# Optimization experiments

Hardware: AMD Instinct MI355X
Metric: run time of the kernel (lower is better)

Reference implementation:

```python
import jax, jax.numpy as jnp
import numpy as np

B, S, D, H, DFF = 2, 2048, 1024, 16, 4096
DK = D // H
EPS = float(np.finfo(np.float32).eps)  # torch RMSNorm default eps = finfo eps


def rmsnorm(x, g):
    var = jnp.mean(x * x, axis=-1, keepdims=True)
    return x * jax.lax.rsqrt(var + EPS) * g


def rope_cos_sin(seq_len, dim, base=10000.0):
    inv_freq = 1.0 / (base ** (jnp.arange(0, dim, 2, dtype=jnp.float32) / dim))
    t = jnp.arange(seq_len, dtype=jnp.float32)
    freqs = jnp.outer(t, inv_freq)            # [S, dim/2]
    emb = jnp.concatenate([freqs, freqs], -1)  # [S, dim]
    return jnp.cos(emb), jnp.sin(emb)


def rotate_half(x):
    x1, x2 = x[..., : x.shape[-1] // 2], x[..., x.shape[-1] // 2:]
    return jnp.concatenate([-x2, x1], axis=-1)


def setup_inputs() -> dict:
    key = jax.random.key(0)
    ks = jax.random.split(key, 16)
    sc = 0.02
    return {
        "x": jax.random.normal(ks[0], (B, S, D), jnp.float32),
        "wq": jax.random.normal(ks[1], (D, D), jnp.float32) * sc,
        "bq": jnp.zeros((D,), jnp.float32),
        "wk": jax.random.normal(ks[2], (D, D), jnp.float32) * sc,
        "bk": jnp.zeros((D,), jnp.float32),
        "wv": jax.random.normal(ks[3], (D, D), jnp.float32) * sc,
        "bv": jnp.zeros((D,), jnp.float32),
        "wo": jax.random.normal(ks[4], (D, D), jnp.float32) * sc,
        "bo": jnp.zeros((D,), jnp.float32),
        "w1": jax.random.normal(ks[5], (D, DFF), jnp.float32) * sc,
        "b1": jnp.zeros((DFF,), jnp.float32),
        "w2": jax.random.normal(ks[6], (DFF, D), jnp.float32) * sc,
        "b2": jnp.zeros((D,), jnp.float32),
        "g1": jnp.ones((D,), jnp.float32),
        "g2": jnp.ones((D,), jnp.float32),
    }


def reference(x, wq, bq, wk, bk, wv, bv, wo, bo, w1, b1, w2, b2, g1, g2):
    b, s, d = x.shape
    # --- self-attention sublayer (pre-RMSNorm residual) ---
    h = rmsnorm(x, g1)
    q = (h @ wq + bq).reshape(b, s, H, DK).transpose(0, 2, 1, 3)  # [B,H,S,dk]
    k = (h @ wk + bk).reshape(b, s, H, DK).transpose(0, 2, 1, 3)
    v = (h @ wv + bv).reshape(b, s, H, DK).transpose(0, 2, 1, 3)
    cos, sin = rope_cos_sin(s, DK)
    cos = cos[None, None]  # [1,1,S,dk]
    sin = sin[None, None]
    q = q * cos + rotate_half(q) * sin
    k = k * cos + rotate_half(k) * sin
    scores = jnp.einsum("bhqd,bhkd->bhqk", q, k) / jnp.sqrt(jnp.float32(DK))
    p = jax.nn.softmax(scores, axis=-1)
    o = jnp.einsum("bhqk,bhkd->bhqd", p, v)
    o = o.transpose(0, 2, 1, 3).reshape(b, s, d)
    attn_out = o @ wo + bo
    x = x + attn_out
    # --- feed-forward sublayer ---
    h2 = rmsnorm(x, g2)
    ff = jax.nn.relu(h2 @ w1 + b1) @ w2 + b2
    return x + ff
```

## Files before the change

### kernel.cpp

```cpp
#include <hip/hip_runtime.h>
#include <math.h>

typedef unsigned short u16;
typedef __attribute__((ext_vector_type(8))) short bf16x8;
typedef __attribute__((ext_vector_type(4))) float f32x4;
typedef __attribute__((ext_vector_type(4))) unsigned int u32x4;

#define B_ 2
#define S_ 2048
#define D_ 1024
#define H_ 16
#define DK_ 64
#define DFF_ 4096
#define EPS_ 1.1920928955078125e-07f
#define EXP2SC 0.18033688011112042f

__device__ __forceinline__ float bf2f(u16 u) {
  unsigned int v = ((unsigned int)u) << 16;
  return __builtin_bit_cast(float, v);
}
__device__ __forceinline__ u16 f2bf(float f) {
  unsigned int x = __builtin_bit_cast(unsigned int, f);
  x += 0x7fffu + ((x >> 16) & 1u);
  return (u16)(x >> 16);
}

typedef __attribute__((address_space(3))) unsigned int lds_uint;
typedef const __attribute__((address_space(1))) unsigned int glb_uint;
__device__ __forceinline__ void gload16(const void* g, void* l) {
  __builtin_amdgcn_global_load_lds((glb_uint*)g, (lds_uint*)l, 16, 0, 0);
}

__device__ __forceinline__ unsigned int cvtpk(float lo, float hi) {
  unsigned int d;
  asm("v_cvt_pk_bf16_f32 %0, %1, %2" : "=v"(d) : "v"(lo), "v"(hi));
  return d;
}
__device__ __forceinline__ void plswap32(unsigned int& a, unsigned int& b) {
  asm("v_permlane32_swap_b32 %0, %1" : "+v"(a), "+v"(b));
}
__device__ __forceinline__ void plswap16(unsigned int& a, unsigned int& b) {
  asm("v_permlane16_swap_b32 %0, %1" : "+v"(a), "+v"(b));
}

__global__ __launch_bounds__(256) void rope_table(float* __restrict__ cosT,
                                                  float* __restrict__ sinT) {
  int idx = blockIdx.x * 256 + threadIdx.x;
  if (idx >= S_ * 32) return;
  int s = idx >> 5, i = idx & 31;
  double inv = exp(((double)(-2 * i) / (double)DK_) * log(10000.0));
  double ang = (double)s * inv;
  cosT[idx] = (float)cos(ang);
  sinT[idx] = (float)sin(ang);
}

__global__ __launch_bounds__(256) void convertT(const float* __restrict__ src,
                                                u16* __restrict__ dst, int R, int C) {
  __shared__ float t[32][33];
  int c0 = blockIdx.x * 32, r0 = blockIdx.y * 32;
  int tx = threadIdx.x, ty = threadIdx.y;
#pragma unroll
  for (int i = 0; i < 32; i += 8)
    t[ty + i][tx] = src[(size_t)(r0 + ty + i) * C + (c0 + tx)];
  __syncthreads();
#pragma unroll
  for (int i = 0; i < 32; i += 8)
    dst[(size_t)(c0 + ty + i) * R + (r0 + tx)] = f2bf(t[tx][ty + i]);
}

__global__ __launch_bounds__(256) void rmsnorm_k(const float* __restrict__ X,
                                                 const float* __restrict__ g,
                                                 u16* __restrict__ out) {
  const int row = blockIdx.x;
  const float* xr = X + (size_t)row * D_;
  u16* orow = out + (size_t)row * D_;
  const int tid = threadIdx.x;
  float vals[4];
  float s = 0.f;
#pragma unroll
  for (int j = 0; j < 4; j++) {
    float v = xr[tid + j * 256];
    vals[j] = v;
    s += v * v;
  }
#pragma unroll
  for (int off = 32; off > 0; off >>= 1) s += __shfl_down(s, off, 64);
  __shared__ float red[4];
  __shared__ float ssc;
  int lane = tid & 63, wave = tid >> 6;
  if (lane == 0) red[wave] = s;
  __syncthreads();
  if (tid == 0) ssc = 1.0f / sqrtf((red[0] + red[1] + red[2] + red[3]) * (1.0f / D_) + EPS_);
  __syncthreads();
  float sc = ssc;
#pragma unroll
  for (int j = 0; j < 4; j++) {
    int i = tid + j * 256;
    orow[i] = f2bf(vals[j] * sc * g[i]);
  }
}

#define GEMM_KLOOP(APTR, BPTR, KLEN, KLD)                                              \
  for (int k0 = 0; k0 < (KLEN); k0 += 64) {                                            \
    _Pragma("unroll")                                                                  \
    for (int p = 0; p < 2; p++) {                                                      \
      _Pragma("unroll")                                                                \
      for (int c = wave; c < BM / 16; c += 4) {                                        \
        const u16* gp = (APTR) + (size_t)(m0 + c * 16 + lrow) * (KLD) + k0 + p * 32 + lcol; \
        gload16(gp, (char*)As + __builtin_amdgcn_readfirstlane(p * (BM * 64) + c * 1024)); \
      }                                                                                \
      _Pragma("unroll")                                                                \
      for (int c = wave; c < BN / 16; c += 4) {                                        \
        const u16* gp = (BPTR) + (size_t)(n0 + c * 16 + lrow) * (KLD) + k0 + p * 32 + lcol; \
        gload16(gp, (char*)Bs + __builtin_amdgcn_readfirstlane(p * (BN * 64) + c * 1024)); \
      }                                                                                \
    }                                                                                  \
    __syncthreads();                                                                   \
    _Pragma("unroll")                                                                  \
    for (int p = 0; p < 2; p++) {                                                      \
      bf16x8 af[WR], bfv[WC];                                                          \
      _Pragma("unroll")                                                                \
      for (int i = 0; i < WR; i++)                                                     \
        af[i] = *(const bf16x8*)&As[p * (BM * 32) + (wm + i * 16 + l16) * 32 + quad * 8]; \
      _Pragma("unroll")                                                                \
      for (int j = 0; j < WC; j++)                                                     \
        bfv[j] = *(const bf16x8*)&Bs[p * (BN * 32) + (wn + j * 16 + l16) * 32 + quad * 8]; \
      _Pragma("unroll")                                                                \
      for (int i = 0; i < WR; i++)                                                     \
        _Pragma("unroll")                                                              \
        for (int j = 0; j < WC; j++)                                                   \
          acc[i][j] = __builtin_amdgcn_mfma_f32_16x16x32_bf16(af[i], bfv[j], acc[i][j], 0, 0, 0); \
    }                                                                                  \
    __syncthreads();                                                                   \
  }

template <int MODE, int WR, int WC>
__global__ __launch_bounds__(256) void gemm_bt(
    const u16* __restrict__ A, const u16* __restrict__ Bt, const float* __restrict__ bias,
    u16* __restrict__ outB, float* __restrict__ outF, const float* __restrict__ resF,
    int M, int N, int K) {
  constexpr int BM = 2 * WR * 16;
  constexpr int BN = 2 * WC * 16;
  __shared__ u16 As[BM * 64];
  __shared__ u16 Bs[BN * 64];
  const int tid = threadIdx.x;
  const int wave = tid >> 6, lane = tid & 63, quad = lane >> 4, l16 = lane & 15;
  const int wm = (wave >> 1) * (WR * 16), wn = (wave & 1) * (WC * 16);
  const int m0 = blockIdx.y * BM, n0 = blockIdx.x * BN;
  const int lrow = lane >> 2, lcol = (lane & 3) * 8;
  f32x4 acc[WR][WC] = {};
  GEMM_KLOOP(A, Bt, K, K)
#pragma unroll
  for (int i = 0; i < WR; i++)
#pragma unroll
    for (int j = 0; j < WC; j++) {
      int col = n0 + wn + j * 16 + l16;
      float bv = bias[col];
#pragma unroll
      for (int r = 0; r < 4; r++) {
        int row = m0 + wm + i * 16 + quad * 4 + r;
        size_t off = (size_t)row * N + col;
        float v = acc[i][j][r] + bv;
        if constexpr (MODE == 1) v = fmaxf(v, 0.f);
        if constexpr (MODE == 2) outF[off] = v + resF[off];
        else outB[off] = f2bf(v);
      }
    }
}

__global__ __launch_bounds__(256) void gemm_qkv(
    const u16* __restrict__ A, const u16* __restrict__ Bt,
    const float* __restrict__ bq, const float* __restrict__ bk, const float* __restrict__ bv,
    const float* __restrict__ cosT, const float* __restrict__ sinT,
    u16* __restrict__ Qb, u16* __restrict__ Kb, u16* __restrict__ VT, int M, int K) {
  constexpr int WR = 4, WC = 4;
  constexpr int BM = 128, BN = 128;
  __shared__ u16 As[BM * 64];
  __shared__ u16 Bs[BN * 64];
  const int tid = threadIdx.x;
  const int wave = tid >> 6, lane = tid & 63, quad = lane >> 4, l16 = lane & 15;
  const int wm = (wave >> 1) * 64, wn = (wave & 1) * 64;
  const int m0 = blockIdx.y * BM, n0 = blockIdx.x * BN;
  const int lrow = lane >> 2, lcol = (lane & 3) * 8;
  f32x4 acc[WR][WC] = {};
  GEMM_KLOOP(A, Bt, K, K)
  const int g = n0 >> 10;
  if (g < 2) {
    u16* dst = (g == 0) ? Qb : Kb;
    const float* bias = (g == 0) ? bq : bk;
    const float scq = (g == 0) ? EXP2SC : 1.0f;
#pragma unroll
    for (int i = 0; i < WR; i++)
#pragma unroll
      for (int jp = 0; jp < 2; jp++) {
        int col0 = n0 + wn + jp * 16 + l16;
        int c0 = col0 & 1023;
        float bv0 = bias[c0], bv1 = bias[c0 + 32];
        int irot = jp * 16 + l16;
        int row0 = m0 + wm + i * 16 + quad * 4;
#pragma unroll
        for (int r = 0; r < 4; r++) {
          int row = row0 + r;
          int s2 = row & 2047;
          float cs = cosT[s2 * 32 + irot];
          float sn = sinT[s2 * 32 + irot];
          float x0 = acc[i][jp][r] + bv0;
          float x1 = acc[i][jp + 2][r] + bv1;
          dst[(size_t)row * D_ + c0]      = f2bf((x0 * cs - x1 * sn) * scq);
          dst[(size_t)row * D_ + c0 + 32] = f2bf((x1 * cs + x0 * sn) * scq);
        }
      }
  } else {
#pragma unroll
    for (int i = 0; i < WR; i++)
#pragma unroll
      for (int j = 0; j < WC; j++) {
        int col = n0 + wn + j * 16 + l16;
        int c = col & 1023;
        float bvv = bv[c];
        int row0 = m0 + wm + i * 16 + quad * 4;
        int hh = c >> 6, dk = c & 63;
        int b = row0 >> 11, s2 = row0 & 2047;
        ushort4 pv;
        pv.x = f2bf(acc[i][j][0] + bvv);
        pv.y = f2bf(acc[i][j][1] + bvv);
        pv.z = f2bf(acc[i][j][2] + bvv);
        pv.w = f2bf(acc[i][j][3] + bvv);
        *(ushort4*)&VT[(((size_t)(b * H_ + hh)) * DK_ + dk) * S_ + s2] = pv;
      }
  }
}

template <int WR, int WC>
__global__ __launch_bounds__(256) void gemm_splitk(
    const u16* __restrict__ A, const u16* __restrict__ Bt, const float* __restrict__ bias,
    float* outF, int M, int N, int Kslice, int Kld) {
  constexpr int BM = 2 * WR * 16;
  constexpr int BN = 2 * WC * 16;
  __shared__ u16 As[BM * 64];
  __shared__ u16 Bs[BN * 64];
  const int tid = threadIdx.x;
  const int wave = tid >> 6, lane = tid & 63, quad = lane >> 4, l16 = lane & 15;
  const int wm = (wave >> 1) * (WR * 16), wn = (wave & 1) * (WC * 16);
  const int m0 = blockIdx.y * BM, n0 = blockIdx.x * BN;
  const int lrow = lane >> 2, lcol = (lane & 3) * 8;
  const u16* Ao = A + (size_t)blockIdx.z * Kslice;
  const u16* Bo = Bt + (size_t)blockIdx.z * Kslice;
  f32x4 acc[WR][WC] = {};
  GEMM_KLOOP(Ao, Bo, Kslice, Kld)
  const bool addb = (blockIdx.z == 0);
#pragma unroll
  for (int i = 0; i < WR; i++)
#pragma unroll
    for (int j = 0; j < WC; j++) {
      int col = n0 + wn + j * 16 + l16;
      float bv = addb ? bias[col] : 0.f;
#pragma unroll
      for (int r = 0; r < 4; r++) {
        int row = m0 + wm + i * 16 + quad * 4 + r;
        unsafeAtomicAdd(&outF[(size_t)row * N + col], acc[i][j][r] + bv);
      }
    }
}

__device__ __forceinline__ void softmax_pack(f32x4 s0, f32x4 s1, f32x4 s2, f32x4 s3,
                                             bf16x8& pf0, bf16x8& pf1) {
  f32x4 p0, p1, p2, p3;
#pragma unroll
  for (int r = 0; r < 4; r++) {
    p0[r] = exp2f(s0[r]);
    p1[r] = exp2f(s1[r]);
    p2[r] = exp2f(s2[r]);
    p3[r] = exp2f(s3[r]);
  }
  unsigned int X0 = cvtpk(p0[0], p0[1]), X1 = cvtpk(p0[2], p0[3]);
  unsigned int Y0 = cvtpk(p1[0], p1[1]), Y1 = cvtpk(p1[2], p1[3]);
  unsigned int Z0 = cvtpk(p2[0], p2[1]), Z1 = cvtpk(p2[2], p2[3]);
  unsigned int W0 = cvtpk(p3[0], p3[1]), W1 = cvtpk(p3[2], p3[3]);
  plswap32(X0, Y0); plswap16(X0, Y0);
  plswap32(X1, Y1); plswap16(X1, Y1);
  plswap32(Z0, W0); plswap16(Z0, W0);
  plswap32(Z1, W1); plswap16(Z1, W1);
  u32x4 lo = {X0, X1, Y0, Y1};
  u32x4 hi = {Z0, Z1, W0, W1};
  pf0 = __builtin_bit_cast(bf16x8, lo);
  pf1 = __builtin_bit_cast(bf16x8, hi);
}

__global__ __launch_bounds__(256, 2) void flash_attn(u16* __restrict__ Q,
                                                     const u16* __restrict__ Kg,
                                                     const u16* __restrict__ VT) {
  const int bh = blockIdx.y;
  const int b = bh >> 4, h = bh & 15;
  const int q0 = blockIdx.x * 128;
  const int tid = threadIdx.x;
  const int wave = tid >> 6, lane = tid & 63, quad = lane >> 4, l16 = lane & 15;
  const size_t base = (size_t)b * S_ * D_ + h * DK_;
  const size_t vbase = (size_t)bh * DK_ * S_;

  __shared__ u16 Ks[2][8192];
  __shared__ u16 Vts[2][8192];

  const int kkey = wave * 32 + (lane >> 3);
  const int kcol = ((lane & 7) ^ (lane >> 3)) * 8;
  const u16* kp0 = Kg + base + (size_t)kkey * D_ + kcol;
  const int vdk0 = wave * 16 + (lane >> 4);
  const int vsel = lane & 15;
  const u16* vp0 = VT + vbase + (size_t)vdk0 * S_;

#define STAGE(BU, KT)                                                                  \
  _Pragma("unroll")                                                                    \
  for (int c = 0; c < 4; c++) {                                                        \
    gload16(kp0 + (size_t)((KT) + c * 8) * D_,                                         \
            (char*)Ks + __builtin_amdgcn_readfirstlane((BU) * 16384 + wave * 4096 + c * 1024)); \
    int vdk = vdk0 + c * 4;                                                            \
    gload16(vp0 + (size_t)(c * 4) * S_ + (KT) + ((vsel ^ (vdk & 7)) * 8),              \
            (char*)Vts + __builtin_amdgcn_readfirstlane((BU) * 16384 + wave * 4096 + c * 1024)); \
  }

  STAGE(0, 0)

  const size_t qoffA = base + (size_t)(q0 + wave * 32 + l16) * D_ + quad * 8;
  const size_t qoffB = qoffA + (size_t)16 * D_;
  bf16x8 qa0 = *(const bf16x8*)(Q + qoffA);
  bf16x8 qa1 = *(const bf16x8*)(Q + qoffA + 32);
  bf16x8 qb0 = *(const bf16x8*)(Q + qoffB);
  bf16x8 qb1 = *(const bf16x8*)(Q + qoffB + 32);

  f32x4 oa[4] = {}, ob[4] = {};
  f32x4 lsa_acc = {}, lsb_acc = {};
  const u32x4 onesu = {0x3F803F80u, 0x3F803F80u, 0x3F803F80u, 0x3F803F80u};
  const bf16x8 ones = __builtin_bit_cast(bf16x8, onesu);
  const int sw = (l16 & 7) << 4;

#define TILE(BU)                                                                       \
  {                                                                                    \
    const char* KsB = (const char*)Ks + (BU) * 16384;                                  \
    const char* VtsB = (const char*)Vts + (BU) * 16384;                                \
    f32x4 sa[2][4] = {}, sb[2][4] = {};                                                \
    __builtin_amdgcn_s_setprio(1);                                                     \
    _Pragma("unroll")                                                                  \
    for (int half = 0; half < 2; half++) {                                             \
      _Pragma("unroll")                                                                \
      for (int nt = 0; nt < 4; nt++) {                                                 \
        const int kr = half * 64 + nt * 16 + l16;                                      \
        const char* krow = KsB + kr * 128;                                             \
        bf16x8 k0 = *(const bf16x8*)(krow + ((quad * 16) ^ sw));                       \
        bf16x8 k1 = *(const bf16x8*)(krow + ((64 + quad * 16) ^ sw));                  \
        sa[half][nt] = __builtin_amdgcn_mfma_f32_16x16x32_bf16(k0, qa0, sa[half][nt], 0, 0, 0); \
        sa[half][nt] = __builtin_amdgcn_mfma_f32_16x16x32_bf16(k1, qa1, sa[half][nt], 0, 0, 0); \
        sb[half][nt] = __builtin_amdgcn_mfma_f32_16x16x32_bf16(k0, qb0, sb[half][nt], 0, 0, 0); \
        sb[half][nt] = __builtin_amdgcn_mfma_f32_16x16x32_bf16(k1, qb1, sb[half][nt], 0, 0, 0); \
      }                                                                                \
    }                                                                                  \
    __builtin_amdgcn_s_setprio(0);                                                     \
    bf16x8 pa[2][2], pb[2][2];                                                         \
    _Pragma("unroll")                                                                  \
    for (int half = 0; half < 2; half++) {                                             \
      softmax_pack(sa[half][0], sa[half][1], sa[half][2], sa[half][3], pa[half][0], pa[half][1]); \
      softmax_pack(sb[half][0], sb[half][1], sb[half][2], sb[half][3], pb[half][0], pb[half][1]); \
    }                                                                                  \
    __builtin_amdgcn_s_setprio(1);                                                     \
    _Pragma("unroll")                                                                  \
    for (int half = 0; half < 2; half++) {                                             \
      lsa_acc = __builtin_amdgcn_mfma_f32_16x16x32_bf16(pa[half][0], ones, lsa_acc, 0, 0, 0); \
      lsa_acc = __builtin_amdgcn_mfma_f32_16x16x32_bf16(pa[half][1], ones, lsa_acc, 0, 0, 0); \
      lsb_acc = __builtin_amdgcn_mfma_f32_16x16x32_bf16(pb[half][0], ones, lsb_acc, 0, 0, 0); \
      lsb_acc = __builtin_amdgcn_mfma_f32_16x16x32_bf16(pb[half][1], ones, lsb_acc, 0, 0, 0); \
      _Pragma("unroll")                                                                \
      for (int nt = 0; nt < 4; nt++) {                                                 \
        const int vr = nt * 16 + l16;                                                  \
        const char* vrow = VtsB + vr * 256;                                            \
        bf16x8 v0 = *(const bf16x8*)(vrow + ((half * 128 + quad * 16) ^ sw));          \
        bf16x8 v1 = *(const bf16x8*)(vrow + ((half * 128 + 64 + quad * 16) ^ sw));     \
        oa[nt] = __builtin_amdgcn_mfma_f32_16x16x32_bf16(pa[half][0], v0, oa[nt], 0, 0, 0); \
        oa[nt] = __builtin_amdgcn_mfma_f32_16x16x32_bf16(pa[half][1], v1, oa[nt], 0, 0, 0); \
        ob[nt] = __builtin_amdgcn_mfma_f32_16x16x32_bf16(pb[half][0], v0, ob[nt], 0, 0, 0); \
        ob[nt] = __builtin_amdgcn_mfma_f32_16x16x32_bf16(pb[half][1], v1, ob[nt], 0, 0, 0); \
      }                                                                                \
    }                                                                                  \
    __builtin_amdgcn_s_setprio(0);                                                     \
  }

  for (int kt = 0; kt < S_; kt += 256) {
    __syncthreads();
    STAGE(1, kt + 128)
    TILE(0)
    __syncthreads();
    if (kt + 256 < S_) { STAGE(0, kt + 256) }
    TILE(1)
  }
#undef STAGE
#undef TILE

#pragma unroll
  for (int r = 0; r < 4; r++) {
    float inva = 1.0f / lsa_acc[r];
    float invb = 1.0f / lsb_acc[r];
    const size_t aoff = base + (size_t)(q0 + wave * 32 + quad * 4 + r) * D_;
    const size_t boff = aoff + (size_t)16 * D_;
#pragma unroll
    for (int nt = 0; nt < 4; nt++) {
      Q[aoff + nt * 16 + l16] = f2bf(oa[nt][r] * inva);
      Q[boff + nt * 16 + l16] = f2bf(ob[nt][r] * invb);
    }
  }
}

extern "C" void kernel_launch(void* const* d_in, const int* in_sizes, int n_in,
                              void* d_out, int out_size, void* d_ws, size_t ws_size,
                              hipStream_t stream) {
  const float* x  = (const float*)d_in[0];
  const float* wq = (const float*)d_in[1];
  const float* bq = (const float*)d_in[2];
  const float* wk = (const float*)d_in[3];
  const float* bk = (const float*)d_in[4];
  const float* wv = (const float*)d_in[5];
  const float* bv = (const float*)d_in[6];
  const float* wo = (const float*)d_in[7];
  const float* bo = (const float*)d_in[8];
  const float* w1 = (const float*)d_in[9];
  const float* b1 = (const float*)d_in[10];
  const float* w2 = (const float*)d_in[11];
  const float* b2 = (const float*)d_in[12];
  const float* g1 = (const float*)d_in[13];
  const float* g2 = (const float*)d_in[14];

  char* ws = (char*)d_ws;
  const size_t MB = 1024 * 1024;
  u16* qkvT = (u16*)(ws + 0 * MB);
  u16* woT  = (u16*)(ws + 6 * MB);
  u16* h    = (u16*)(ws + 8 * MB);
  u16* Qb   = (u16*)(ws + 16 * MB);
  u16* Kb   = (u16*)(ws + 24 * MB);
  float* cosT = (float*)(ws + 32 * MB);
  float* sinT = (float*)(ws + 32 * MB + 256 * 1024);
  u16* w2T  = (u16*)(ws + 0 * MB);
  u16* w1T  = (u16*)(ws + 16 * MB);
  u16* f1   = (u16*)(ws + 24 * MB);
  u16* h2   = h;
  u16* Ob   = Qb;
  u16* VT   = (u16*)d_out;
  float* x2 = (float*)d_out;
  const bool bigffn = (ws_size >= 57 * MB);

  const int MS = B_ * S_;
  dim3 tb32(32, 8);
  rope_table<<<(S_ * 32 + 255) / 256, 256, 0, stream>>>(cosT, sinT);
  convertT<<<dim3(32, 32), tb32, 0, stream>>>(wq, qkvT, D_, D_);
  convertT<<<dim3(32, 32), tb32, 0, stream>>>(wk, qkvT + (size_t)D_ * D_, D_, D_);
  convertT<<<dim3(32, 32), tb32, 0, stream>>>(wv, qkvT + 2 * (size_t)D_ * D_, D_, D_);
  convertT<<<dim3(32, 32), tb32, 0, stream>>>(wo, woT, D_, D_);

  rmsnorm_k<<<MS, 256, 0, stream>>>(x, g1, h);
  gemm_qkv<<<dim3(3 * D_ / 128, MS / 128), 256, 0, stream>>>(h, qkvT, bq, bk, bv, cosT, sinT, Qb, Kb, VT, MS, D_);
  flash_attn<<<dim3(S_ / 128, B_ * H_), 256, 0, stream>>>(Qb, Kb, VT);
  gemm_bt<2, 4, 2><<<dim3(D_ / 64, MS / 128), 256, 0, stream>>>(Ob, woT, bo, nullptr, x2, x, MS, D_, D_);

  convertT<<<dim3(DFF_ / 32, D_ / 32), tb32, 0, stream>>>(w1, w1T, D_, DFF_);
  convertT<<<dim3(D_ / 32, DFF_ / 32), tb32, 0, stream>>>(w2, w2T, DFF_, D_);
  rmsnorm_k<<<MS, 256, 0, stream>>>(x2, g2, h2);
  if (bigffn) {
    gemm_bt<1, 4, 4><<<dim3(DFF_ / 128, MS / 128), 256, 0, stream>>>(h2, w1T, b1, f1, nullptr, nullptr, MS, DFF_, D_);
    gemm_splitk<4, 2><<<dim3(D_ / 64, MS / 128, 2), 256, 0, stream>>>(f1, w2T, b2, x2, MS, D_, 2048, DFF_);
  } else {
    for (int i = 0; i < 2; i++) {
      const u16* h2h = h2 + (size_t)i * 2048 * D_;
      float* x2h = x2 + (size_t)i * 2048 * D_;
      gemm_bt<1, 4, 4><<<dim3(DFF_ / 128, 2048 / 128), 256, 0, stream>>>(h2h, w1T, b1, f1, nullptr, nullptr, 2048, DFF_, D_);
      gemm_splitk<4, 2><<<dim3(D_ / 64, 2048 / 128, 2), 256, 0, stream>>>(f1, w2T, b2, x2h, 2048, D_, 2048, DFF_);
    }
  }
  (void)in_sizes; (void)n_in; (void)out_size;
}
```

Before: 381.6 us.

## Merge weight-prep launches, add XCD swizzle to GEMMs, widen split-K tiles

Folds the four QKV/O weight transposes and the RoPE table into one launch, and the w1/w2 transposes into another, which cuts the number of kernel launches. All GEMM kernels remap block indices so that neighbouring tiles land on the same XCD, aiming for better L2 reuse. The FFN down-projection split-K GEMM moves from 128x64 to 128x128 tiles, which halves its block count and raises per-block register use.

```diff
diff --git a/kernel.cpp b/kernel.cpp
--- a/kernel.cpp
+++ b/kernel.cpp
@@ -43,29 +43,74 @@
   asm("v_permlane16_swap_b32 %0, %1" : "+v"(a), "+v"(b));
 }
 
-__global__ __launch_bounds__(256) void rope_table(float* __restrict__ cosT,
-                                                  float* __restrict__ sinT) {
-  int idx = blockIdx.x * 256 + threadIdx.x;
-  if (idx >= S_ * 32) return;
-  int s = idx >> 5, i = idx & 31;
-  double inv = exp(((double)(-2 * i) / (double)DK_) * log(10000.0));
-  double ang = (double)s * inv;
-  cosT[idx] = (float)cos(ang);
-  sinT[idx] = (float)sin(ang);
-}
-
-__global__ __launch_bounds__(256) void convertT(const float* __restrict__ src,
-                                                u16* __restrict__ dst, int R, int C) {
+__device__ __forceinline__ void xcd_swizzle(int& bx, int& by) {
+  const int nx = gridDim.x;
+  const int nwg = nx * gridDim.y;
+  const int lin = blockIdx.y * nx + blockIdx.x;
+  const int swz = (lin & 7) * (nwg >> 3) + (lin >> 3);
+  bx = swz % nx;
+  by = swz / nx;
+}
+
+__global__ __launch_bounds__(256) void prep_qkvo(
+    const float* __restrict__ wq, const float* __restrict__ wk,
+    const float* __restrict__ wv, const float* __restrict__ wo,
+    u16* __restrict__ qkvT, u16* __restrict__ woT,
+    float* __restrict__ cosT, float* __restrict__ sinT) {
   __shared__ float t[32][33];
-  int c0 = blockIdx.x * 32, r0 = blockIdx.y * 32;
-  int tx = threadIdx.x, ty = threadIdx.y;
-#pragma unroll
-  for (int i = 0; i < 32; i += 8)
-    t[ty + i][tx] = src[(size_t)(r0 + ty + i) * C + (c0 + tx)];
-  __syncthreads();
-#pragma unroll
-  for (int i = 0; i < 32; i += 8)
-    dst[(size_t)(c0 + ty + i) * R + (r0 + tx)] = f2bf(t[tx][ty + i]);
+  const int bid = blockIdx.x;
+  const int tid = threadIdx.x;
+  if (bid < 4096) {
+    const int m = bid >> 10;
+    const int tb = bid & 1023;
+    const float* src = (m == 0) ? wq : (m == 1) ? wk : (m == 2) ? wv : wo;
+    u16* dst = (m == 3) ? woT : qkvT + (size_t)m * D_ * D_;
+    const int c0 = (tb & 31) * 32, r0 = (tb >> 5) * 32;
+    const int tx = tid & 31, ty = tid >> 5;
+#pragma unroll
+    for (int i = 0; i < 32; i += 8)
+      t[ty + i][tx] = src[(size_t)(r0 + ty + i) * D_ + (c0 + tx)];
+    __syncthreads();
+#pragma unroll
+    for (int i = 0; i < 32; i += 8)
+      dst[(size_t)(c0 + ty + i) * D_ + (r0 + tx)] = f2bf(t[tx][ty + i]);
+  } else {
+    const int idx = (bid - 4096) * 256 + tid;
+    const int s = idx >> 5, i = idx & 31;
+    double inv = exp(((double)(-2 * i) / (double)DK_) * log(10000.0));
+    double ang = (double)s * inv;
+    cosT[idx] = (float)cos(ang);
+    sinT[idx] = (float)sin(ang);
+  }
+}
+
+__global__ __launch_bounds__(256) void prep_w12(
+    const float* __restrict__ w1, const float* __restrict__ w2,
+    u16* __restrict__ w1T, u16* __restrict__ w2T) {
+  __shared__ float t[32][33];
+  const int bid = blockIdx.x;
+  const int tid = threadIdx.x;
+  const int tx = tid & 31, ty = tid >> 5;
+  if (bid < 4096) {
+    const int c0 = (bid & 127) * 32, r0 = (bid >> 7) * 32;
+#pragma unroll
+    for (int i = 0; i < 32; i += 8)
+      t[ty + i][tx] = w1[(size_t)(r0 + ty + i) * DFF_ + (c0 + tx)];
+    __syncthreads();
+#pragma unroll
+    for (int i = 0; i < 32; i += 8)
+      w1T[(size_t)(c0 + ty + i) * D_ + (r0 + tx)] = f2bf(t[tx][ty + i]);
+  } else {
+    const int b2 = bid - 4096;
+    const int c0 = (b2 & 31) * 32, r0 = (b2 >> 5) * 32;
+#pragma unroll
+    for (int i = 0; i < 32; i += 8)
+      t[ty + i][tx] = w2[(size_t)(r0 + ty + i) * D_ + (c0 + tx)];
+    __syncthreads();
+#pragma unroll
+    for (int i = 0; i < 32; i += 8)
+      w2T[(size_t)(c0 + ty + i) * DFF_ + (r0 + tx)] = f2bf(t[tx][ty + i]);
+  }
 }
 
 __global__ __launch_bounds__(256) void rmsnorm_k(const float* __restrict__ X,
@@ -146,7 +191,9 @@
   const int tid = threadIdx.x;
   const int wave = tid >> 6, lane = tid & 63, quad = lane >> 4, l16 = lane & 15;
   const int wm = (wave >> 1) * (WR * 16), wn = (wave & 1) * (WC * 16);
-  const int m0 = blockIdx.y * BM, n0 = blockIdx.x * BN;
+  int bx, by;
+  xcd_swizzle(bx, by);
+  const int m0 = by * BM, n0 = bx * BN;
   const int lrow = lane >> 2, lcol = (lane & 3) * 8;
   f32x4 acc[WR][WC] = {};
   GEMM_KLOOP(A, Bt, K, K)
@@ -180,7 +227,9 @@
   const int tid = threadIdx.x;
   const int wave = tid >> 6, lane = tid & 63, quad = lane >> 4, l16 = lane & 15;
   const int wm = (wave >> 1) * 64, wn = (wave & 1) * 64;
-  const int m0 = blockIdx.y * BM, n0 = blockIdx.x * BN;
+  int bx, by;
+  xcd_swizzle(bx, by);
+  const int m0 = by * BM, n0 = bx * BN;
   const int lrow = lane >> 2, lcol = (lane & 3) * 8;
   f32x4 acc[WR][WC] = {};
   GEMM_KLOOP(A, Bt, K, K)
@@ -242,7 +291,9 @@
   const int tid = threadIdx.x;
   const int wave = tid >> 6, lane = tid & 63, quad = lane >> 4, l16 = lane & 15;
   const int wm = (wave >> 1) * (WR * 16), wn = (wave & 1) * (WC * 16);
-  const int m0 = blockIdx.y * BM, n0 = blockIdx.x * BN;
+  int bx, by;
+  xcd_swizzle(bx, by);
+  const int m0 = by * BM, n0 = bx * BN;
   const int lrow = lane >> 2, lcol = (lane & 3) * 8;
   const u16* Ao = A + (size_t)blockIdx.z * Kslice;
   const u16* Bo = Bt + (size_t)blockIdx.z * Kslice;
@@ -445,30 +496,23 @@
   const bool bigffn = (ws_size >= 57 * MB);
 
   const int MS = B_ * S_;
-  dim3 tb32(32, 8);
-  rope_table<<<(S_ * 32 + 255) / 256, 256, 0, stream>>>(cosT, sinT);
-  convertT<<<dim3(32, 32), tb32, 0, stream>>>(wq, qkvT, D_, D_);
-  convertT<<<dim3(32, 32), tb32, 0, stream>>>(wk, qkvT + (size_t)D_ * D_, D_, D_);
-  convertT<<<dim3(32, 32), tb32, 0, stream>>>(wv, qkvT + 2 * (size_t)D_ * D_, D_, D_);
-  convertT<<<dim3(32, 32), tb32, 0, stream>>>(wo, woT, D_, D_);
-
+  prep_qkvo<<<4096 + S_ * 32 / 256, 256, 0, stream>>>(wq, wk, wv, wo, qkvT, woT, cosT, sinT);
   rmsnorm_k<<<MS, 256, 0, stream>>>(x, g1, h);
   gemm_qkv<<<dim3(3 * D_ / 128, MS / 128), 256, 0, stream>>>(h, qkvT, bq, bk, bv, cosT, sinT, Qb, Kb, VT, MS, D_);
   flash_attn<<<dim3(S_ / 128, B_ * H_), 256, 0, stream>>>(Qb, Kb, VT);
   gemm_bt<2, 4, 2><<<dim3(D_ / 64, MS / 128), 256, 0, stream>>>(Ob, woT, bo, nullptr, x2, x, MS, D_, D_);
 
-  convertT<<<dim3(DFF_ / 32, D_ / 32), tb32, 0, stream>>>(w1, w1T, D_, DFF_);
-  convertT<<<dim3(D_ / 32, DFF_ / 32), tb32, 0, stream>>>(w2, w2T, DFF_, D_);
+  prep_w12<<<8192, 256, 0, stream>>>(w1, w2, w1T, w2T);
   rmsnorm_k<<<MS, 256, 0, stream>>>(x2, g2, h2);
   if (bigffn) {
     gemm_bt<1, 4, 4><<<dim3(DFF_ / 128, MS / 128), 256, 0, stream>>>(h2, w1T, b1, f1, nullptr, nullptr, MS, DFF_, D_);
-    gemm_splitk<4, 2><<<dim3(D_ / 64, MS / 128, 2), 256, 0, stream>>>(f1, w2T, b2, x2, MS, D_, 2048, DFF_);
+    gemm_splitk<4, 4><<<dim3(D_ / 128, MS / 128, 2), 256, 0, stream>>>(f1, w2T, b2, x2, MS, D_, 2048, DFF_);
   } else {
     for (int i = 0; i < 2; i++) {
       const u16* h2h = h2 + (size_t)i * 2048 * D_;
       float* x2h = x2 + (size_t)i * 2048 * D_;
       gemm_bt<1, 4, 4><<<dim3(DFF_ / 128, 2048 / 128), 256, 0, stream>>>(h2h, w1T, b1, f1, nullptr, nullptr, 2048, DFF_, D_);
-      gemm_splitk<4, 2><<<dim3(D_ / 64, 2048 / 128, 2), 256, 0, stream>>>(f1, w2T, b2, x2h, 2048, D_, 2048, DFF_);
+      gemm_splitk<4, 4><<<dim3(D_ / 128, 2048 / 128, 2), 256, 0, stream>>>(f1, w2T, b2, x2h, 2048, D_, 2048, DFF_);
     }
   }
   (void)in_sizes; (void)n_in; (void)out_size;
```

New measurement: 373.9 us. 1.02x faster.
